# Kernel optimization log

Measured on AMD Instinct MI355X. Metric: run time of the kernel, lower is better.

## Reference

```python
import jax, jax.numpy as jnp
import numpy as np


def dct_matrix(N: int) -> jnp.ndarray:
    # Orthonormal DCT-II matrix: D[k, n] = s_k * cos(pi*(2n+1)k / (2N))
    n = jnp.arange(N, dtype=jnp.float32)
    k = jnp.arange(N, dtype=jnp.float32)[:, None]
    D = jnp.cos(jnp.pi * (2.0 * n + 1.0) * k / (2.0 * N))
    scale = jnp.where(k == 0, jnp.sqrt(1.0 / N), jnp.sqrt(2.0 / N))
    return D * scale


def setup_inputs() -> dict:
    key = jax.random.key(0)
    k1, k2, k3 = jax.random.split(key, 3)
    B, C, H, W = 16, 128, 128, 128
    top_k, red = 16, 4
    x = jax.random.normal(k1, (B, C, H, W), dtype=jnp.float32)
    w1 = jax.random.normal(k2, (top_k, top_k // red), dtype=jnp.float32) * (1.0 / np.sqrt(top_k))
    b1 = jnp.zeros((top_k // red,), dtype=jnp.float32)
    w2 = jax.random.normal(k3, (top_k // red, 1), dtype=jnp.float32) * (1.0 / np.sqrt(top_k // red))
    b2 = jnp.zeros((1,), dtype=jnp.float32)
    return {"x": x, "w1": w1, "b1": b1, "w2": w2, "b2": b2}


def reference(x, w1, b1, w2, b2):
    B, C, H, W = x.shape
    top_k = w1.shape[0]
    # dct_energy uses x.detach() in the original -> no grad through this path
    xs = jax.lax.stop_gradient(x)
    DH = dct_matrix(H)
    DW = dct_matrix(W)
    # 2D orthonormal DCT-II via two matmuls: DH @ x @ DW^T
    t = jnp.einsum('hH,bcHW->bchW', DH, xs)
    dct2 = jnp.einsum('bchW,wW->bchw', t, DW)
    energy = jnp.abs(dct2).mean(axis=1).reshape(B, H * W)  # [B, H*W]
    topk_vals, _ = jax.lax.top_k(energy, top_k)  # [B, top_k], descending
    h = jax.nn.relu(topk_vals @ w1 + b1)
    att = jax.nn.sigmoid(h @ w2 + b2)  # [B, 1]
    return x * att[:, :, None, None]
```

## Files before the change

### kernel.cpp

```cpp
#include <hip/hip_runtime.h>


typedef __attribute__((ext_vector_type(8))) _Float16 half8;
typedef __attribute__((ext_vector_type(16))) float f32x16;

#define NCH 32
#define CPB 4

#define Z16 {0.f,0.f,0.f,0.f,0.f,0.f,0.f,0.f,0.f,0.f,0.f,0.f,0.f,0.f,0.f,0.f}

#define SWZ(row, c) (((((row) * 128 + (c)) * 2)) ^ (((row) & 7) << 4))

__device__ __forceinline__ unsigned short f2h(float f) {
    union { _Float16 h; unsigned short u; } cv;
    cv.h = (_Float16)f;
    return cv.u;
}
__device__ __forceinline__ unsigned int pack2(float a, float b) {
    return (unsigned int)f2h(a) | ((unsigned int)f2h(b) << 16);
}

__global__ __launch_bounds__(256) void dct_prep(unsigned short* __restrict__ Dm) {
    int i = blockIdx.x * 256 + threadIdx.x;
    int k = i >> 7, n = i & 127;
    float s = (k == 0) ? 0.08838834764831845f : 0.125f;
    float ang = (float)((2 * n + 1) * k) * 0.012271846303085130f;
    Dm[i] = f2h(s * cosf(ang));
}

__global__ __launch_bounds__(512) void dct_energy_kernel(
    const float* __restrict__ x, const unsigned short* __restrict__ Dm,
    float* __restrict__ energy, float* __restrict__ partial)
{
    __shared__ __attribute__((aligned(16))) unsigned short Xs[128 * 128];
    __shared__ __attribute__((aligned(16))) unsigned short Ps[128 * 128];

    const int b = blockIdx.x;
    const int chunk = blockIdx.y;
    const int tid = threadIdx.x;
    const int lane = tid & 63;
    const int wid = tid >> 6;
    const int wm = wid >> 1;
    const int wn = wid & 1;
    const int l31 = lane & 31;
    const int hi = lane >> 5;

    const float4* xb4 = (const float4*)(x + (((size_t)(b * 128 + chunk * CPB)) << 14));

    float en0[16], en1[16];
#pragma unroll
    for (int r = 0; r < 16; ++r) { en0[r] = 0.f; en1[r] = 0.f; }

    const int rowX = 32 * wm + l31;
    const int k2a = 64 * wn + l31;
    const int dOffA0 = k2a * 128;
    const int dOffA1 = (k2a + 32) * 128;
    const int dOffB = (32 * wm + l31) * 128;

    float4 ld[8];
#pragma unroll
    for (int i = 0; i < 8; ++i) ld[i] = xb4[i * 512 + tid];
#pragma unroll
    for (int i = 0; i < 8; ++i) {
        int fidx = i * 512 + tid;
        int row = fidx >> 5, c = (fidx & 31) << 2;
        uint2 v; v.x = pack2(ld[i].x, ld[i].y); v.y = pack2(ld[i].z, ld[i].w);
        *(uint2*)((char*)Xs + SWZ(row, c)) = v;
    }
    __syncthreads();

    for (int s = 0; s < CPB; ++s) {
        if (s + 1 < CPB) {
            const float4* nx = xb4 + ((size_t)(s + 1) << 12);
#pragma unroll
            for (int i = 0; i < 8; ++i) ld[i] = nx[i * 512 + tid];
        }

        f32x16 acc0 = Z16, acc1 = Z16;
#pragma unroll
        for (int kk = 0; kk < 8; ++kk) {
            int c0 = kk * 16 + hi * 8;
            half8 aX = *(const half8*)((const char*)Xs + SWZ(rowX, c0));
            half8 bD0 = *(const half8*)(const void*)(Dm + dOffA0 + c0);
            half8 bD1 = *(const half8*)(const void*)(Dm + dOffA1 + c0);
            acc0 = __builtin_amdgcn_mfma_f32_32x32x16_f16(aX, bD0, acc0, 0, 0, 0);
            acc1 = __builtin_amdgcn_mfma_f32_32x32x16_f16(aX, bD1, acc1, 0, 0, 0);
        }
#pragma unroll
        for (int g = 0; g < 4; ++g) {
            int h0 = 32 * wm + 8 * g + 4 * hi;
            uint2 v0; v0.x = pack2(acc0[4 * g + 0], acc0[4 * g + 1]);
            v0.y = pack2(acc0[4 * g + 2], acc0[4 * g + 3]);
            *(uint2*)((char*)Ps + SWZ(k2a, h0)) = v0;
            uint2 v1; v1.x = pack2(acc1[4 * g + 0], acc1[4 * g + 1]);
            v1.y = pack2(acc1[4 * g + 2], acc1[4 * g + 3]);
            *(uint2*)((char*)Ps + SWZ(k2a + 32, h0)) = v1;
        }
        __syncthreads();

        f32x16 d0 = Z16, d1 = Z16;
#pragma unroll
        for (int kk = 0; kk < 8; ++kk) {
            int c0 = kk * 16 + hi * 8;
            half8 aD = *(const half8*)(const void*)(Dm + dOffB + c0);
            half8 bP0 = *(const half8*)((const char*)Ps + SWZ(k2a, c0));
            half8 bP1 = *(const half8*)((const char*)Ps + SWZ(k2a + 32, c0));
            d0 = __builtin_amdgcn_mfma_f32_32x32x16_f16(aD, bP0, d0, 0, 0, 0);
            d1 = __builtin_amdgcn_mfma_f32_32x32x16_f16(aD, bP1, d1, 0, 0, 0);
        }
#pragma unroll
        for (int r = 0; r < 16; ++r) { en0[r] += fabsf(d0[r]); en1[r] += fabsf(d1[r]); }

        if (s + 1 < CPB) {
#pragma unroll
            for (int i = 0; i < 8; ++i) {
                int fidx = i * 512 + tid;
                int row = fidx >> 5, c = (fidx & 31) << 2;
                uint2 v; v.x = pack2(ld[i].x, ld[i].y); v.y = pack2(ld[i].z, ld[i].w);
                *(uint2*)((char*)Xs + SWZ(row, c)) = v;
            }
        }
        __syncthreads();
    }

    if (partial) {
        float* pb = partial + (((size_t)(b * NCH + chunk)) << 14);
#pragma unroll
        for (int r = 0; r < 16; ++r) {
            int row = 32 * wm + (r & 3) + 8 * (r >> 2) + 4 * hi;
            int idx = row * 128 + k2a;
            pb[idx] = en0[r];
            pb[idx + 32] = en1[r];
        }
    } else {
        float* eb = energy + ((size_t)b << 14);
#pragma unroll
        for (int r = 0; r < 16; ++r) {
            int row = 32 * wm + (r & 3) + 8 * (r >> 2) + 4 * hi;
            int idx = row * 128 + k2a;
            atomicAdd(&eb[idx], en0[r]);
            atomicAdd(&eb[idx + 32], en1[r]);
        }
    }
}

__global__ __launch_bounds__(256) void reduce_energy(
    const float* __restrict__ partial, float* __restrict__ energy)
{
    int g = blockIdx.x * 256 + threadIdx.x;
    int b = g >> 14, i = g & 16383;
    const float* p = partial + (((size_t)b * NCH) << 14) + i;
    float s = 0.f;
#pragma unroll
    for (int ch = 0; ch < NCH; ++ch) s += p[(size_t)ch << 14];
    energy[g] = s;
}

__global__ __launch_bounds__(256) void topk_mlp(
    const float* __restrict__ energy,
    const float* __restrict__ w1, const float* __restrict__ b1,
    const float* __restrict__ w2, const float* __restrict__ b2,
    float* __restrict__ att)
{
    __shared__ float red[256];
    __shared__ int redi[256];
    __shared__ float topv[16];
    int b = blockIdx.x, t = threadIdx.x;
    const float* eb = energy + ((size_t)b << 14);

    float v[64];
#pragma unroll
    for (int k = 0; k < 64; ++k) v[k] = eb[k * 256 + t];
    unsigned long long mask = ~0ull;

    for (int j = 0; j < 16; ++j) {
        float mv = -1e30f; int mk = 0;
#pragma unroll
        for (int k = 0; k < 64; ++k) {
            float c = ((mask >> k) & 1ull) ? v[k] : -1e30f;
            if (c > mv) { mv = c; mk = k; }
        }
        red[t] = mv; redi[t] = mk * 256 + t;
        __syncthreads();
        for (int s = 128; s > 0; s >>= 1) {
            if (t < s && red[t + s] > red[t]) { red[t] = red[t + s]; redi[t] = redi[t + s]; }
            __syncthreads();
        }
        int widx = redi[0];
        float wval = red[0];
        if (t == (widx & 255)) mask &= ~(1ull << (widx >> 8));
        if (t == 0) topv[j] = wval * (1.0f / 128.0f);
        __syncthreads();
    }

    if (t == 0) {
        float z = b2[0];
#pragma unroll
        for (int jj = 0; jj < 4; ++jj) {
            float a = b1[jj];
#pragma unroll
            for (int i = 0; i < 16; ++i) a += topv[i] * w1[i * 4 + jj];
            a = fmaxf(a, 0.0f);
            z += a * w2[jj];
        }
        att[b] = 1.0f / (1.0f + expf(-z));
    }
}

__global__ __launch_bounds__(256) void scale_kernel(
    const float4* __restrict__ x4, const float* __restrict__ att,
    float4* __restrict__ out4, int n4)
{
    int i = blockIdx.x * 256 + threadIdx.x;
    int stride = gridDim.x * 256;
    for (; i < n4; i += stride) {
        float a = att[i >> 19];
        float4 v = x4[i];
        v.x *= a; v.y *= a; v.z *= a; v.w *= a;
        out4[i] = v;
    }
}

extern "C" void kernel_launch(void* const* d_in, const int* in_sizes, int n_in,
                              void* d_out, int out_size, void* d_ws, size_t ws_size,
                              hipStream_t stream) {
    const float* x  = (const float*)d_in[0];
    const float* w1 = (const float*)d_in[1];
    const float* b1 = (const float*)d_in[2];
    const float* w2 = (const float*)d_in[3];
    const float* b2 = (const float*)d_in[4];

    char* wsb = (char*)d_ws;
    unsigned short* Dm = (unsigned short*)wsb;
    float* energy = (float*)(wsb + (1 << 15));
    float* att    = (float*)(wsb + (1 << 15) + (1 << 20));
    float* partial = (float*)(wsb + (1 << 21));
    size_t need_partial = (size_t)(1 << 21) + (size_t)16 * NCH * 16384 * 4;
    bool use_partial = (ws_size >= need_partial);

    dct_prep<<<64, 256, 0, stream>>>(Dm);
    if (!use_partial) hipMemsetAsync(energy, 0, (size_t)16 * 16384 * 4, stream);

    dim3 g2(16, NCH);
    dct_energy_kernel<<<g2, 512, 0, stream>>>(x, Dm, energy,
                                              use_partial ? partial : (float*)nullptr);
    if (use_partial) reduce_energy<<<1024, 256, 0, stream>>>(partial, energy);

    topk_mlp<<<16, 256, 0, stream>>>(energy, w1, b1, w2, b2, att);
    scale_kernel<<<2048, 256, 0, stream>>>((const float4*)x, att,
                                           (float4*)d_out, out_size / 4);
}
```

Baseline: 359.0 us.

## Pre-swizzle DCT matrix for coalesced MFMA loads and use wave-shuffle top-k

The DCT matrix is now written in a fragment-packed layout indexed by (kk, hi, row, j), so each MFMA operand load from global memory reads contiguous 16-byte chunks across lanes instead of strided rows. Separately, the top-k kernel moves to 1024 threads with 16 values per thread and uses wavefront shuffles plus a small cross-wave pass, replacing the shared-memory tree reduction that needed many barriers per selected element. The intent is to cut uncoalesced D-matrix traffic in the DCT kernel and shorten the serial top-k selection. Ties are broken by value only, so the order among equal values may differ, which does not change the selected values.

```diff
diff --git a/kernel.cpp b/kernel.cpp
--- a/kernel.cpp
+++ b/kernel.cpp
@@ -20,16 +20,17 @@
     return (unsigned int)f2h(a) | ((unsigned int)f2h(b) << 16);
 }
 
-__global__ __launch_bounds__(256) void dct_prep(unsigned short* __restrict__ Dm) {
+__global__ __launch_bounds__(256) void dct_prep(unsigned short* __restrict__ Dp) {
     int i = blockIdx.x * 256 + threadIdx.x;
-    int k = i >> 7, n = i & 127;
-    float s = (k == 0) ? 0.08838834764831845f : 0.125f;
-    float ang = (float)((2 * n + 1) * k) * 0.012271846303085130f;
-    Dm[i] = f2h(s * cosf(ang));
+    int j = i & 7, r = (i >> 3) & 127, hi = (i >> 10) & 1, kk = i >> 11;
+    int c = kk * 16 + hi * 8 + j;
+    float s = (r == 0) ? 0.08838834764831845f : 0.125f;
+    float ang = (float)((2 * c + 1) * r) * 0.012271846303085130f;
+    Dp[i] = f2h(s * cosf(ang));
 }
 
 __global__ __launch_bounds__(512) void dct_energy_kernel(
-    const float* __restrict__ x, const unsigned short* __restrict__ Dm,
+    const float* __restrict__ x, const unsigned short* __restrict__ Dp,
     float* __restrict__ energy, float* __restrict__ partial)
 {
     __shared__ __attribute__((aligned(16))) unsigned short Xs[128 * 128];
@@ -53,9 +54,9 @@
 
     const int rowX = 32 * wm + l31;
     const int k2a = 64 * wn + l31;
-    const int dOffA0 = k2a * 128;
-    const int dOffA1 = (k2a + 32) * 128;
-    const int dOffB = (32 * wm + l31) * 128;
+    const unsigned short* dB0 = Dp + k2a * 8;
+    const unsigned short* dB1 = Dp + (k2a + 32) * 8;
+    const unsigned short* dA  = Dp + rowX * 8;
 
     float4 ld[8];
 #pragma unroll
@@ -80,9 +81,10 @@
 #pragma unroll
         for (int kk = 0; kk < 8; ++kk) {
             int c0 = kk * 16 + hi * 8;
+            int kb = (kk * 2 + hi) << 10;
             half8 aX = *(const half8*)((const char*)Xs + SWZ(rowX, c0));
-            half8 bD0 = *(const half8*)(const void*)(Dm + dOffA0 + c0);
-            half8 bD1 = *(const half8*)(const void*)(Dm + dOffA1 + c0);
+            half8 bD0 = *(const half8*)(const void*)(dB0 + kb);
+            half8 bD1 = *(const half8*)(const void*)(dB1 + kb);
             acc0 = __builtin_amdgcn_mfma_f32_32x32x16_f16(aX, bD0, acc0, 0, 0, 0);
             acc1 = __builtin_amdgcn_mfma_f32_32x32x16_f16(aX, bD1, acc1, 0, 0, 0);
         }
@@ -102,7 +104,8 @@
 #pragma unroll
         for (int kk = 0; kk < 8; ++kk) {
             int c0 = kk * 16 + hi * 8;
-            half8 aD = *(const half8*)(const void*)(Dm + dOffB + c0);
+            int kb = (kk * 2 + hi) << 10;
+            half8 aD = *(const half8*)(const void*)(dA + kb);
             half8 bP0 = *(const half8*)((const char*)Ps + SWZ(k2a, c0));
             half8 bP1 = *(const half8*)((const char*)Ps + SWZ(k2a + 32, c0));
             d0 = __builtin_amdgcn_mfma_f32_32x32x16_f16(aD, bP0, d0, 0, 0, 0);
@@ -156,41 +159,54 @@
     energy[g] = s;
 }
 
-__global__ __launch_bounds__(256) void topk_mlp(
+__global__ __launch_bounds__(1024) void topk_mlp(
     const float* __restrict__ energy,
     const float* __restrict__ w1, const float* __restrict__ b1,
     const float* __restrict__ w2, const float* __restrict__ b2,
     float* __restrict__ att)
 {
-    __shared__ float red[256];
-    __shared__ int redi[256];
+    __shared__ float wv[16];
+    __shared__ int   wi[16];
+    __shared__ float winv_s;
+    __shared__ int   wini_s;
     __shared__ float topv[16];
     int b = blockIdx.x, t = threadIdx.x;
+    int lane = t & 63, wid = t >> 6;
     const float* eb = energy + ((size_t)b << 14);
 
-    float v[64];
-#pragma unroll
-    for (int k = 0; k < 64; ++k) v[k] = eb[k * 256 + t];
-    unsigned long long mask = ~0ull;
+    float v[16];
+#pragma unroll
+    for (int k = 0; k < 16; ++k) v[k] = eb[k * 1024 + t];
+    unsigned mask = 0xFFFFu;
 
     for (int j = 0; j < 16; ++j) {
-        float mv = -1e30f; int mk = 0;
-#pragma unroll
-        for (int k = 0; k < 64; ++k) {
-            float c = ((mask >> k) & 1ull) ? v[k] : -1e30f;
-            if (c > mv) { mv = c; mk = k; }
-        }
-        red[t] = mv; redi[t] = mk * 256 + t;
-        __syncthreads();
-        for (int s = 128; s > 0; s >>= 1) {
-            if (t < s && red[t + s] > red[t]) { red[t] = red[t + s]; redi[t] = redi[t + s]; }
-            __syncthreads();
-        }
-        int widx = redi[0];
-        float wval = red[0];
-        if (t == (widx & 255)) mask &= ~(1ull << (widx >> 8));
-        if (t == 0) topv[j] = wval * (1.0f / 128.0f);
-        __syncthreads();
+        float mv = -1e30f; int mi = 0;
+#pragma unroll
+        for (int k = 0; k < 16; ++k) {
+            if ((mask >> k) & 1u) {
+                float c = v[k];
+                if (c > mv) { mv = c; mi = k * 1024 + t; }
+            }
+        }
+#pragma unroll
+        for (int off = 32; off >= 1; off >>= 1) {
+            float ov = __shfl_down(mv, off);
+            int   oi = __shfl_down(mi, off);
+            if (ov > mv) { mv = ov; mi = oi; }
+        }
+        if (lane == 0) { wv[wid] = mv; wi[wid] = mi; }
+        __syncthreads();
+        if (t == 0) {
+            float bv = wv[0]; int bi = wi[0];
+#pragma unroll
+            for (int w = 1; w < 16; ++w)
+                if (wv[w] > bv) { bv = wv[w]; bi = wi[w]; }
+            winv_s = bv; wini_s = bi;
+            topv[j] = bv * (1.0f / 128.0f);
+        }
+        __syncthreads();
+        int gw = wini_s;
+        if (t == (gw & 1023)) mask &= ~(1u << (gw >> 10));
     }
 
     if (t == 0) {
@@ -231,22 +247,22 @@
     const float* b2 = (const float*)d_in[4];
 
     char* wsb = (char*)d_ws;
-    unsigned short* Dm = (unsigned short*)wsb;
+    unsigned short* Dp = (unsigned short*)wsb;
     float* energy = (float*)(wsb + (1 << 15));
     float* att    = (float*)(wsb + (1 << 15) + (1 << 20));
     float* partial = (float*)(wsb + (1 << 21));
     size_t need_partial = (size_t)(1 << 21) + (size_t)16 * NCH * 16384 * 4;
     bool use_partial = (ws_size >= need_partial);
 
-    dct_prep<<<64, 256, 0, stream>>>(Dm);
+    dct_prep<<<64, 256, 0, stream>>>(Dp);
     if (!use_partial) hipMemsetAsync(energy, 0, (size_t)16 * 16384 * 4, stream);
 
     dim3 g2(16, NCH);
-    dct_energy_kernel<<<g2, 512, 0, stream>>>(x, Dm, energy,
+    dct_energy_kernel<<<g2, 512, 0, stream>>>(x, Dp, energy,
                                               use_partial ? partial : (float*)nullptr);
     if (use_partial) reduce_energy<<<1024, 256, 0, stream>>>(partial, energy);
 
-    topk_mlp<<<16, 256, 0, stream>>>(energy, w1, b1, w2, b2, att);
+    topk_mlp<<<16, 1024, 0, stream>>>(energy, w1, b1, w2, b2, att);
     scale_kernel<<<2048, 256, 0, stream>>>((const float4*)x, att,
                                            (float4*)d_out, out_size / 4);
 }
```

Result: faster. 318.3 us (-11.3%).
